# Performance work log

Hardware: AMD Instinct MI355X
Metric: run time of the kernel (lower is better)

## Reference

```python
import jax, jax.numpy as jnp
import numpy as np

B, S, D, H = 2, 2048, 1024, 16
DK = D // H


def setup_inputs() -> dict:
    key = jax.random.key(0)
    ks = jax.random.split(key, 10)
    ws = 1.0 / np.sqrt(D)  # realistic linear-layer init scale
    return {
        "q": jax.random.normal(ks[0], (B, S, D), jnp.float32),
        "k": jax.random.normal(ks[1], (B, S, D), jnp.float32),
        "v": jax.random.normal(ks[2], (B, S, D), jnp.float32),
        "mask": jnp.tril(jnp.ones((1, 1, S, S), jnp.int32)),  # causal mask, 0 = blocked
        "max_seq_len": S,
        "Wq": jax.random.normal(ks[3], (D, D), jnp.float32) * ws,
        "bq": jnp.zeros((D,), jnp.float32),
        "Wk": jax.random.normal(ks[4], (D, D), jnp.float32) * ws,
        "bk": jnp.zeros((D,), jnp.float32),
        "Wv": jax.random.normal(ks[5], (D, D), jnp.float32) * ws,
        "bv": jnp.zeros((D,), jnp.float32),
        "Wo": jax.random.normal(ks[6], (D, D), jnp.float32) * ws,
        "bo": jnp.zeros((D,), jnp.float32),
    }


def _rope(x, sin, cos):
    # x: [B, H, S, DK]; sin/cos: [S, DK//2] -> pairwise rotation of (even, odd) lanes
    b, h, s, dk = x.shape
    x2 = x.reshape(b, h, s, dk // 2, 2)
    x0, x1 = x2[..., 0], x2[..., 1]
    r0 = x0 * cos - x1 * sin
    r1 = x0 * sin + x1 * cos
    return jnp.stack([r0, r1], axis=-1).reshape(b, h, s, dk)


def reference(q, k, v, mask, max_seq_len, Wq, bq, Wk, bk, Wv, bv, Wo, bo):
    b, s, d = q.shape
    lin = lambda x, W, bias: x @ W.T + bias  # torch nn.Linear convention
    split = lambda x: x.reshape(b, s, H, DK).transpose(0, 2, 1, 3)  # [B,H,S,DK]
    qh = split(lin(q, Wq, bq))
    kh = split(lin(k, Wk, bk))
    vh = split(lin(v, Wv, bv))

    # rotary position embeddings (applied since max_seq_len is given)
    inv_freq = 10000.0 ** (-2.0 * jnp.arange(0, DK, 2, dtype=jnp.float32) / DK)  # [DK//2]
    pos = jnp.arange(s, dtype=jnp.float32)
    ang = pos[:, None] * inv_freq[None, :]  # [S, DK//2]
    sin, cos = jnp.sin(ang), jnp.cos(ang)
    qh = _rope(qh, sin, cos)
    kh = _rope(kh, sin, cos)

    scale = 1.0 / jnp.sqrt(jnp.float32(DK))
    scores = jnp.einsum("bhqd,bhkd->bhqk", qh, kh) * scale
    scores = jnp.where(mask == 0, jnp.float32(-1e9), scores)
    attn = jax.nn.softmax(scores, axis=-1)
    ctx = jnp.einsum("bhqk,bhkd->bhqd", attn, vh)
    ctx = ctx.transpose(0, 2, 1, 3).reshape(b, s, d)
    return ctx @ Wo.T + bo
```

## Files before the change

kernel.cpp:

```cpp
#include <hip/hip_runtime.h>

#define S_LEN 2048
#define D_MODEL 1024
#define NH 16
#define BATCH 2
#define M_TOK 4096

typedef _Float16 f16;
typedef __attribute__((ext_vector_type(8))) _Float16 f16x8;
typedef __attribute__((ext_vector_type(4))) _Float16 f16x4;
typedef __attribute__((ext_vector_type(4))) float f32x4;
typedef __attribute__((ext_vector_type(16))) float f32x16;
typedef __attribute__((ext_vector_type(2))) unsigned int uint2v;

__device__ __forceinline__ void gl_lds16(const f16* g, f16* l) {
  __builtin_amdgcn_global_load_lds(
      (const __attribute__((address_space(1))) void*)g,
      (__attribute__((address_space(3))) void*)l, 16, 0, 0);
}

__global__ void cvt_all_kernel(
    const float* __restrict__ q, const float* __restrict__ k, const float* __restrict__ v,
    const float* __restrict__ Wq, const float* __restrict__ Wk,
    const float* __restrict__ Wv, const float* __restrict__ Wo,
    f16* __restrict__ qb, f16* __restrict__ kb, f16* __restrict__ vb,
    f16* __restrict__ Wqh, f16* __restrict__ Wkh, f16* __restrict__ Wvh,
    f16* __restrict__ Woh) {
  const int NX = (M_TOK * D_MODEL) / 4;
  const int NW = (D_MODEL * D_MODEL) / 4;
  const int total = 3 * NX + 4 * NW;
  int stride = gridDim.x * blockDim.x;
  for (int i = blockIdx.x * blockDim.x + threadIdx.x; i < total; i += stride) {
    const float* src; f16* dst; int off;
    if (i < 3 * NX) {
      int ts = i / NX; off = i - ts * NX;
      src = ts == 0 ? q : ts == 1 ? k : v;
      dst = ts == 0 ? qb : ts == 1 ? kb : vb;
    } else {
      int j = i - 3 * NX;
      int ts = j / NW; off = j - ts * NW;
      src = ts == 0 ? Wq : ts == 1 ? Wk : ts == 2 ? Wv : Wo;
      dst = ts == 0 ? Wqh : ts == 1 ? Wkh : ts == 2 ? Wvh : Woh;
    }
    float4 vv = ((const float4*)src)[off];
    union { f16 h[4]; uint2 u; } o;
    o.h[0] = (f16)vv.x; o.h[1] = (f16)vv.y; o.h[2] = (f16)vv.z; o.h[3] = (f16)vv.w;
    ((uint2*)dst)[off] = o.u;
  }
}

__global__ void rope_table_kernel(float* __restrict__ sin_t, float* __restrict__ cos_t) {
  int idx = blockIdx.x * blockDim.x + threadIdx.x;
  int s = idx >> 5, i = idx & 31;
  float inv = powf(10000.0f, -(float)i * (1.0f / 16.0f));
  float ang = (float)s * inv;
  sin_t[idx] = sinf(ang);
  cos_t[idx] = cosf(ang);
}


__global__ __launch_bounds__(256) void qkv_gemm_kernel(
    const f16* __restrict__ qb, const f16* __restrict__ kb, const f16* __restrict__ vb,
    const f16* __restrict__ Wqh, const f16* __restrict__ Wkh, const f16* __restrict__ Wvh,
    const float* __restrict__ bq, const float* __restrict__ bk, const float* __restrict__ bv,
    f16* __restrict__ Qh, f16* __restrict__ Kt, f16* __restrict__ Vt,
    const float* __restrict__ sin_t, const float* __restrict__ cos_t) {
  constexpr int K = D_MODEL;
  const int z = blockIdx.z;
  const f16* A = z == 0 ? qb : z == 1 ? kb : vb;
  const f16* Bm = z == 0 ? Wqh : z == 1 ? Wkh : Wvh;
  const float* bias = z == 0 ? bq : z == 1 ? bk : bv;

  __shared__ f16 As[2][128 * 32];
  __shared__ f16 Bs[2][128 * 32];
  const int t = threadIdx.x, w = t >> 6, l = t & 63;
  const int bm = blockIdx.x, bn = blockIdx.y;
  const int wr = w >> 1, wc = w & 1;
  const int lr = l & 15;
  const int lkp = (((l >> 4) ^ ((l >> 1) & 3)) * 8);

  f32x4 acc[4][4] = {};

  const int su = (((t & 3) ^ ((t >> 3) & 3)) * 8);
  const f16* gA = A + (size_t)(bm * 128 + (t >> 2)) * K + su;
  const f16* gB = Bm + (size_t)(bn * 128 + (t >> 2)) * K + su;

  auto stage = [&](int buf, int koff) {
    f16* a0 = buf ? &As[1][w * 512] : &As[0][w * 512];
    f16* b0 = buf ? &Bs[1][w * 512] : &Bs[0][w * 512];
    gl_lds16(gA + koff, a0);
    gl_lds16(gA + koff + (size_t)64 * K, a0 + 2048);
    gl_lds16(gB + koff, b0);
    gl_lds16(gB + koff + (size_t)64 * K, b0 + 2048);
  };

  stage(0, 0);
  __syncthreads();
  for (int ti = 0; ti < 32; ++ti) {
    int cur = ti & 1;
    if (ti + 1 < 32) stage(cur ^ 1, (ti + 1) * 32);
    const f16* Ab = cur ? As[1] : As[0];
    const f16* Bb = cur ? Bs[1] : Bs[0];
    f16x8 af[4], bf[4];
#pragma unroll
    for (int m = 0; m < 4; m++) af[m] = *(const f16x8*)&Ab[(wr * 64 + m * 16 + lr) * 32 + lkp];
#pragma unroll
    for (int n = 0; n < 4; n++) bf[n] = *(const f16x8*)&Bb[(wc * 64 + n * 16 + lr) * 32 + lkp];
#pragma unroll
    for (int m = 0; m < 4; m++)
#pragma unroll
      for (int n = 0; n < 4; n++)
        acc[m][n] = __builtin_amdgcn_mfma_f32_16x16x32_f16(af[m], bf[n], acc[m][n], 0, 0, 0);
    __syncthreads();
  }

#pragma unroll
  for (int m = 0; m < 4; m++) {
    int rbase = bm * 128 + wr * 64 + m * 16 + ((l >> 4) << 2);
#pragma unroll
    for (int n = 0; n < 4; n++) {
      int c = bn * 128 + wc * 64 + n * 16 + lr;
      float bv_ = bias[c];
#pragma unroll
      for (int j = 0; j < 4; j++) {
        float x = acc[m][n][j] + bv_;
        int rr = rbase + j;
        int b = rr >> 11, s = rr & (S_LEN - 1);
        int h = c >> 6, dk = c & 63;
        int bh = b * NH + h;
        if (z == 2) {
          Vt[((((size_t)bh * (S_LEN / 16) + (s >> 4)) * 64) + dk) * 16 + (s & 15)] = (f16)x;
        } else {
          float p = __shfl_xor(x, 1);
          float sv = sin_t[s * 32 + (dk >> 1)];
          float cv = cos_t[s * 32 + (dk >> 1)];
          float ov = (dk & 1) ? (p * sv + x * cv) : (x * cv - p * sv);
          if (z == 0) {
            Qh[(((size_t)bh) * S_LEN + s) * 64 + dk] = (f16)ov;
          } else {
            Kt[(((((size_t)bh * 64 + (s >> 5)) * 4 + (dk >> 4)) * 32) + (s & 31)) * 16 + (dk & 15)] = (f16)ov;
          }
        }
      }
    }
  }
}

__global__ __launch_bounds__(256) void out_gemm_kernel(
    const f16* __restrict__ A, const f16* __restrict__ Bm,
    const float* __restrict__ bias, float* __restrict__ Cout) {
  constexpr int N = D_MODEL, K = D_MODEL;
  __shared__ f16 As[2][128 * 32];
  __shared__ f16 Bs[2][128 * 32];
  const int t = threadIdx.x, w = t >> 6, l = t & 63;
  const int bm = blockIdx.x, bn = blockIdx.y;
  const int wr = w >> 1, wc = w & 1;
  const int lr = l & 15;
  const int lkp = (((l >> 4) ^ ((l >> 1) & 3)) * 8);

  f32x4 acc[4][4] = {};

  const int su = (((t & 3) ^ ((t >> 3) & 3)) * 8);
  const f16* gA = A + (size_t)(bm * 128 + (t >> 2)) * K + su;
  const f16* gB = Bm + (size_t)(bn * 128 + (t >> 2)) * K + su;

  auto stage = [&](int buf, int koff) {
    f16* a0 = buf ? &As[1][w * 512] : &As[0][w * 512];
    f16* b0 = buf ? &Bs[1][w * 512] : &Bs[0][w * 512];
    gl_lds16(gA + koff, a0);
    gl_lds16(gA + koff + (size_t)64 * K, a0 + 2048);
    gl_lds16(gB + koff, b0);
    gl_lds16(gB + koff + (size_t)64 * K, b0 + 2048);
  };

  stage(0, 0);
  __syncthreads();
  for (int ti = 0; ti < 32; ++ti) {
    int cur = ti & 1;
    if (ti + 1 < 32) stage(cur ^ 1, (ti + 1) * 32);
    const f16* Ab = cur ? As[1] : As[0];
    const f16* Bb = cur ? Bs[1] : Bs[0];
    f16x8 af[4], bf[4];
#pragma unroll
    for (int m = 0; m < 4; m++) af[m] = *(const f16x8*)&Ab[(wr * 64 + m * 16 + lr) * 32 + lkp];
#pragma unroll
    for (int n = 0; n < 4; n++) bf[n] = *(const f16x8*)&Bb[(wc * 64 + n * 16 + lr) * 32 + lkp];
#pragma unroll
    for (int m = 0; m < 4; m++)
#pragma unroll
      for (int n = 0; n < 4; n++)
        acc[m][n] = __builtin_amdgcn_mfma_f32_16x16x32_f16(af[m], bf[n], acc[m][n], 0, 0, 0);
    __syncthreads();
  }

#pragma unroll
  for (int m = 0; m < 4; m++) {
    int rbase = bm * 128 + wr * 64 + m * 16 + ((l >> 4) << 2);
#pragma unroll
    for (int n = 0; n < 4; n++) {
      int c = bn * 128 + wc * 64 + n * 16 + lr;
      float bv = bias[c];
#pragma unroll
      for (int j = 0; j < 4; j++)
        Cout[(size_t)(rbase + j) * N + c] = acc[m][n][j] + bv;
    }
  }
}

__global__ __launch_bounds__(256, 4) void attn_kernel(
    const f16* __restrict__ Qh, const f16* __restrict__ Kt,
    const f16* __restrict__ Vt, f16* __restrict__ ctx) {
  __shared__ f16 po_lds[2][64][32];
  __shared__ float ml_lds[2][64];
  const int t = threadIdx.x, w = t >> 6, l = t & 63;
  const int lq = l & 31, hi = l >> 5;
  const int id = blockIdx.x;
  const int xcd = id & 7, slot = id >> 3;
  const int bh = (slot >> 5) * 8 + xcd;
  const int b = bh >> 4, h = bh & 15;
  const int cp = slot & 31;
  const int pairidx = w >> 1, wk = w & 1;
  const int cx = pairidx ? (63 - cp) : cp;
  const int q0w = cx * 32;
  const int q = q0w + lq;
  const int ntot = cx + 1;
  const int nA = (ntot + 1) >> 1;
  const int t0 = wk ? nA : 0;
  const int t1 = wk ? ntot : nA;

  const f16* Qb = Qh + ((size_t)bh * S_LEN + q0w) * 64;
  const f16* Kb = Kt + (size_t)bh * S_LEN * 64;
  const f16* Vb = Vt + (size_t)bh * S_LEN * 64;

  f16x8 qf[4];
#pragma unroll
  for (int ks = 0; ks < 4; ks++) {
    qf[ks] = *(const f16x8*)(Qb + (size_t)lq * 64 + ks * 16 + hi * 8);
#pragma unroll
    for (int j = 0; j < 8; j++) qf[ks][j] *= (f16)0.18033688f;
  }

  f32x16 o[2] = {};
  float m = -1e30f, lsum = 0.f;

  auto loadK = [&](int kt, f16x8* dst) {
    const f16* kp = Kb + (size_t)kt * 2048 + lq * 16 + hi * 8;
#pragma unroll
    for (int ks = 0; ks < 4; ks++)
      dst[ks] = *(const f16x8*)(kp + ks * 512);
  };

  auto body = [&](int kt, f16x8* cur, f16x8* nxt) {
    const int k0 = kt * 32;
    loadK(kt + 1 < t1 ? kt + 1 : kt, nxt);
    f32x16 s = {};
#pragma unroll
    for (int ks = 0; ks < 4; ks++)
      s = __builtin_amdgcn_mfma_f32_32x32x16_f16(cur[ks], qf[ks], s, 0, 0, 0);
    const f16* vp = Vb + (size_t)(k0 >> 4) * 1024 + lq * 16 + hi * 8;
    f16x8 vf00 = *(const f16x8*)(vp);
    f16x8 vf10 = *(const f16x8*)(vp + 512);
    f16x8 vf01 = *(const f16x8*)(vp + 1024);
    f16x8 vf11 = *(const f16x8*)(vp + 1536);

    if (kt == cx) {
#pragma unroll
      for (int r = 0; r < 16; r++) {
        int kk = k0 + (r & 3) + 8 * (r >> 2) + 4 * hi;
        if (kk > q) s[r] = -1e30f;
      }
    }
    float a0 = fmaxf(s[0], s[1]), a1 = fmaxf(s[2], s[3]);
    float a2 = fmaxf(s[4], s[5]), a3 = fmaxf(s[6], s[7]);
    float a4 = fmaxf(s[8], s[9]), a5 = fmaxf(s[10], s[11]);
    float a6 = fmaxf(s[12], s[13]), a7 = fmaxf(s[14], s[15]);
    float b0_ = fmaxf(a0, a1), b1_ = fmaxf(a2, a3), b2_ = fmaxf(a4, a5), b3_ = fmaxf(a6, a7);
    float pmax = fmaxf(fmaxf(b0_, b1_), fmaxf(b2_, b3_));
    pmax = fmaxf(pmax, __shfl_xor(pmax, 32));
    if (!__all(pmax <= m + 11.5f)) {
      float mn = fmaxf(m, pmax);
      float sc = exp2f(m - mn);
#pragma unroll
      for (int r = 0; r < 16; r++) { o[0][r] *= sc; o[1][r] *= sc; }
      lsum *= sc;
      m = mn;
    }
#pragma unroll
    for (int r = 0; r < 16; r++) s[r] = exp2f(s[r] - m);
    float c0 = (s[0] + s[1]) + (s[2] + s[3]);
    float c1 = (s[4] + s[5]) + (s[6] + s[7]);
    float c2 = (s[8] + s[9]) + (s[10] + s[11]);
    float c3 = (s[12] + s[13]) + (s[14] + s[15]);
    float rs = (c0 + c1) + (c2 + c3);
    rs += __shfl_xor(rs, 32);
    lsum += rs;

    unsigned pw[8];
#pragma unroll
    for (int i = 0; i < 8; i++)
      pw[i] = __builtin_bit_cast(unsigned, __builtin_amdgcn_cvt_pkrtz(s[2 * i], s[2 * i + 1]));
    uint2v s02 = __builtin_amdgcn_permlane32_swap(pw[0], pw[2], false, false);
    uint2v s13 = __builtin_amdgcn_permlane32_swap(pw[1], pw[3], false, false);
    uint2v s46 = __builtin_amdgcn_permlane32_swap(pw[4], pw[6], false, false);
    uint2v s57 = __builtin_amdgcn_permlane32_swap(pw[5], pw[7], false, false);
    union BU { unsigned u[4]; f16x8 v; };
    BU pb0, pb1;
    pb0.u[0] = s02[0]; pb0.u[1] = s13[0]; pb0.u[2] = s02[1]; pb0.u[3] = s13[1];
    pb1.u[0] = s46[0]; pb1.u[1] = s57[0]; pb1.u[2] = s46[1]; pb1.u[3] = s57[1];

    o[0] = __builtin_amdgcn_mfma_f32_32x32x16_f16(vf00, pb0.v, o[0], 0, 0, 0);
    o[0] = __builtin_amdgcn_mfma_f32_32x32x16_f16(vf01, pb1.v, o[0], 0, 0, 0);
    o[1] = __builtin_amdgcn_mfma_f32_32x32x16_f16(vf10, pb0.v, o[1], 0, 0, 0);
    o[1] = __builtin_amdgcn_mfma_f32_32x32x16_f16(vf11, pb1.v, o[1], 0, 0, 0);
  };

  f16x8 ka[4], kb_[4];
  if (t0 < t1) loadK(t0, ka);
  int kt = t0;
  for (; kt + 2 <= t1; kt += 2) { body(kt, ka, kb_); body(kt + 1, kb_, ka); }
  if (kt < t1) body(kt, ka, kb_);

  if (wk == 1) {
#pragma unroll
    for (int dt = 0; dt < 2; dt++)
#pragma unroll
      for (int r = 0; r < 16; r++)
        po_lds[pairidx][(dt * 16 + r) * 2 + hi][lq] = (f16)o[dt][r];
    if (hi == 0) { ml_lds[pairidx][lq] = m; ml_lds[pairidx][32 + lq] = lsum; }
  }
  __syncthreads();
  if (wk == 0) {
    float mB = ml_lds[pairidx][lq], lB = ml_lds[pairidx][32 + lq];
    float mf = fmaxf(m, mB);
    float sA = exp2f(m - mf), sB = exp2f(mB - mf);
    float lf = lsum * sA + lB * sB;
    float inv = 1.0f / lf;
    f16* crow = ctx + ((size_t)(b * S_LEN + q)) * D_MODEL + h * 64;
#pragma unroll
    for (int dt = 0; dt < 2; dt++) {
#pragma unroll
      for (int g = 0; g < 4; g++) {
        f16x4 ov;
#pragma unroll
        for (int c = 0; c < 4; c++) {
          int r = g * 4 + c;
          float vB = (float)po_lds[pairidx][(dt * 16 + r) * 2 + hi][lq];
          ov[c] = (f16)((o[dt][r] * sA + vB * sB) * inv);
        }
        *(f16x4*)(crow + dt * 32 + g * 8 + hi * 4) = ov;
      }
    }
  }
}

extern "C" void kernel_launch(void* const* d_in, const int* in_sizes, int n_in,
                              void* d_out, int out_size, void* d_ws, size_t ws_size,
                              hipStream_t stream) {
  const float* q = (const float*)d_in[0];
  const float* k = (const float*)d_in[1];
  const float* v = (const float*)d_in[2];
  const float* Wq = (const float*)d_in[5];
  const float* bq = (const float*)d_in[6];
  const float* Wk = (const float*)d_in[7];
  const float* bk = (const float*)d_in[8];
  const float* Wv = (const float*)d_in[9];
  const float* bv = (const float*)d_in[10];
  const float* Wo = (const float*)d_in[11];
  const float* bo = (const float*)d_in[12];

  char* ws = (char*)d_ws;
  const size_t MB = 1ull << 20;
  f16* qb   = (f16*)(ws + 0 * MB);
  f16* kb   = (f16*)(ws + 8 * MB);
  f16* vb   = (f16*)(ws + 16 * MB);
  f16* Wqh  = (f16*)(ws + 24 * MB);
  f16* Wkh  = (f16*)(ws + 26 * MB);
  f16* Wvh  = (f16*)(ws + 28 * MB);
  f16* Woh  = (f16*)(ws + 30 * MB);
  f16* Qh   = (f16*)(ws + 32 * MB);
  f16* Kt   = (f16*)(ws + 40 * MB);
  f16* Vt   = (f16*)(ws + 48 * MB);
  f16* ctxb = (f16*)(ws + 56 * MB);
  float* sin_t = (float*)(ws + 64 * MB);
  float* cos_t = (float*)(ws + 64 * MB + 256 * 1024);

  cvt_all_kernel<<<dim3(2048), dim3(256), 0, stream>>>(
      q, k, v, Wq, Wk, Wv, Wo, qb, kb, vb, Wqh, Wkh, Wvh, Woh);
  rope_table_kernel<<<dim3((S_LEN * 32) / 256), dim3(256), 0, stream>>>(sin_t, cos_t);

  qkv_gemm_kernel<<<dim3(M_TOK / 128, D_MODEL / 128, 3), 256, 0, stream>>>(
      qb, kb, vb, Wqh, Wkh, Wvh, bq, bk, bv, Qh, Kt, Vt, sin_t, cos_t);

  attn_kernel<<<dim3(1024), dim3(256), 0, stream>>>(Qh, Kt, Vt, ctxb);

  out_gemm_kernel<<<dim3(M_TOK / 128, D_MODEL / 128), 256, 0, stream>>>(ctxb, Woh, bo, (float*)d_out);
}
```

Measured before the change: 137.5 us.

## Fuse rope table into convert kernel, vectorize V stores, add MFMA priority hints

The rope sin/cos table is now computed inside the conversion kernel and stored as interleaved float2, which removes one kernel launch and turns two table lookups into one. The V epilogue in the QKV GEMM writes four contiguous halves in a single vector store instead of four scalar stores. The attention kernel wraps its MFMA sections in s_setprio so those waves get scheduling priority over others. Each change is small, and the priority hint may do nothing or upset the interleaving between waves.

```diff
diff --git a/kernel.cpp b/kernel.cpp
--- a/kernel.cpp
+++ b/kernel.cpp
@@ -25,12 +25,19 @@
     const float* __restrict__ Wv, const float* __restrict__ Wo,
     f16* __restrict__ qb, f16* __restrict__ kb, f16* __restrict__ vb,
     f16* __restrict__ Wqh, f16* __restrict__ Wkh, f16* __restrict__ Wvh,
-    f16* __restrict__ Woh) {
+    f16* __restrict__ Woh, float2* __restrict__ rope2) {
   const int NX = (M_TOK * D_MODEL) / 4;
   const int NW = (D_MODEL * D_MODEL) / 4;
   const int total = 3 * NX + 4 * NW;
   int stride = gridDim.x * blockDim.x;
-  for (int i = blockIdx.x * blockDim.x + threadIdx.x; i < total; i += stride) {
+  int tid0 = blockIdx.x * blockDim.x + threadIdx.x;
+  if (tid0 < S_LEN * 32) {
+    int s = tid0 >> 5, i = tid0 & 31;
+    float inv = powf(10000.0f, -(float)i * (1.0f / 16.0f));
+    float ang = (float)s * inv;
+    rope2[tid0] = make_float2(cosf(ang), sinf(ang));
+  }
+  for (int i = tid0; i < total; i += stride) {
     const float* src; f16* dst; int off;
     if (i < 3 * NX) {
       int ts = i / NX; off = i - ts * NX;
@@ -49,22 +56,13 @@
   }
 }
 
-__global__ void rope_table_kernel(float* __restrict__ sin_t, float* __restrict__ cos_t) {
-  int idx = blockIdx.x * blockDim.x + threadIdx.x;
-  int s = idx >> 5, i = idx & 31;
-  float inv = powf(10000.0f, -(float)i * (1.0f / 16.0f));
-  float ang = (float)s * inv;
-  sin_t[idx] = sinf(ang);
-  cos_t[idx] = cosf(ang);
-}
-
 
 __global__ __launch_bounds__(256) void qkv_gemm_kernel(
     const f16* __restrict__ qb, const f16* __restrict__ kb, const f16* __restrict__ vb,
     const f16* __restrict__ Wqh, const f16* __restrict__ Wkh, const f16* __restrict__ Wvh,
     const float* __restrict__ bq, const float* __restrict__ bk, const float* __restrict__ bv,
     f16* __restrict__ Qh, f16* __restrict__ Kt, f16* __restrict__ Vt,
-    const float* __restrict__ sin_t, const float* __restrict__ cos_t) {
+    const float2* __restrict__ rope2) {
   constexpr int K = D_MODEL;
   const int z = blockIdx.z;
   const f16* A = z == 0 ? qb : z == 1 ? kb : vb;
@@ -121,20 +119,26 @@
     for (int n = 0; n < 4; n++) {
       int c = bn * 128 + wc * 64 + n * 16 + lr;
       float bv_ = bias[c];
-#pragma unroll
-      for (int j = 0; j < 4; j++) {
-        float x = acc[m][n][j] + bv_;
-        int rr = rbase + j;
-        int b = rr >> 11, s = rr & (S_LEN - 1);
+      if (z == 2) {
+        int s0 = rbase;
+        int b = s0 >> 11, s = s0 & (S_LEN - 1);
         int h = c >> 6, dk = c & 63;
         int bh = b * NH + h;
-        if (z == 2) {
-          Vt[((((size_t)bh * (S_LEN / 16) + (s >> 4)) * 64) + dk) * 16 + (s & 15)] = (f16)x;
-        } else {
+        f16x4 ov;
+#pragma unroll
+        for (int j = 0; j < 4; j++) ov[j] = (f16)(acc[m][n][j] + bv_);
+        *(f16x4*)&Vt[((((size_t)bh * (S_LEN / 16) + (s >> 4)) * 64) + dk) * 16 + (s & 15)] = ov;
+      } else {
+#pragma unroll
+        for (int j = 0; j < 4; j++) {
+          float x = acc[m][n][j] + bv_;
+          int rr = rbase + j;
+          int b = rr >> 11, s = rr & (S_LEN - 1);
+          int h = c >> 6, dk = c & 63;
+          int bh = b * NH + h;
           float p = __shfl_xor(x, 1);
-          float sv = sin_t[s * 32 + (dk >> 1)];
-          float cv = cos_t[s * 32 + (dk >> 1)];
-          float ov = (dk & 1) ? (p * sv + x * cv) : (x * cv - p * sv);
+          float2 cs = rope2[s * 32 + (dk >> 1)];
+          float ov = (dk & 1) ? (p * cs.y + x * cs.x) : (x * cs.x - p * cs.y);
           if (z == 0) {
             Qh[(((size_t)bh) * S_LEN + s) * 64 + dk] = (f16)ov;
           } else {
@@ -254,9 +258,11 @@
     const int k0 = kt * 32;
     loadK(kt + 1 < t1 ? kt + 1 : kt, nxt);
     f32x16 s = {};
+    __builtin_amdgcn_s_setprio(1);
 #pragma unroll
     for (int ks = 0; ks < 4; ks++)
       s = __builtin_amdgcn_mfma_f32_32x32x16_f16(cur[ks], qf[ks], s, 0, 0, 0);
+    __builtin_amdgcn_s_setprio(0);
     const f16* vp = Vb + (size_t)(k0 >> 4) * 1024 + lq * 16 + hi * 8;
     f16x8 vf00 = *(const f16x8*)(vp);
     f16x8 vf10 = *(const f16x8*)(vp + 512);
@@ -308,10 +314,12 @@
     pb0.u[0] = s02[0]; pb0.u[1] = s13[0]; pb0.u[2] = s02[1]; pb0.u[3] = s13[1];
     pb1.u[0] = s46[0]; pb1.u[1] = s57[0]; pb1.u[2] = s46[1]; pb1.u[3] = s57[1];
 
+    __builtin_amdgcn_s_setprio(1);
     o[0] = __builtin_amdgcn_mfma_f32_32x32x16_f16(vf00, pb0.v, o[0], 0, 0, 0);
     o[0] = __builtin_amdgcn_mfma_f32_32x32x16_f16(vf01, pb1.v, o[0], 0, 0, 0);
     o[1] = __builtin_amdgcn_mfma_f32_32x32x16_f16(vf10, pb0.v, o[1], 0, 0, 0);
     o[1] = __builtin_amdgcn_mfma_f32_32x32x16_f16(vf11, pb1.v, o[1], 0, 0, 0);
+    __builtin_amdgcn_s_setprio(0);
   };
 
   f16x8 ka[4], kb_[4];
@@ -381,15 +389,13 @@
   f16* Kt   = (f16*)(ws + 40 * MB);
   f16* Vt   = (f16*)(ws + 48 * MB);
   f16* ctxb = (f16*)(ws + 56 * MB);
-  float* sin_t = (float*)(ws + 64 * MB);
-  float* cos_t = (float*)(ws + 64 * MB + 256 * 1024);
+  float2* rope2 = (float2*)(ws + 64 * MB);
 
   cvt_all_kernel<<<dim3(2048), dim3(256), 0, stream>>>(
-      q, k, v, Wq, Wk, Wv, Wo, qb, kb, vb, Wqh, Wkh, Wvh, Woh);
-  rope_table_kernel<<<dim3((S_LEN * 32) / 256), dim3(256), 0, stream>>>(sin_t, cos_t);
+      q, k, v, Wq, Wk, Wv, Wo, qb, kb, vb, Wqh, Wkh, Wvh, Woh, rope2);
 
   qkv_gemm_kernel<<<dim3(M_TOK / 128, D_MODEL / 128, 3), 256, 0, stream>>>(
-      qb, kb, vb, Wqh, Wkh, Wvh, bq, bk, bv, Qh, Kt, Vt, sin_t, cos_t);
+      qb, kb, vb, Wqh, Wkh, Wvh, bq, bk, bv, Qh, Kt, Vt, rope2);
 
   attn_kernel<<<dim3(1024), dim3(256), 0, stream>>>(Qh, Kt, Vt, ctxb);
 
```

Measured after the change: 123.1 us. 1.12x faster.
